# Kernel tuning notes

Measured on AMD Instinct MI355X. Metric: run time of the kernel, lower is better.

Reference implementation:

```python
import jax, jax.numpy as jnp
import numpy as np

EPS = 1e-5  # torch BatchNorm2d default eps


def _conv_bn(x, w, b, gamma, beta, mean, var):
    # 1x1 conv -> relu -> BatchNorm (eval mode, running stats), per Conv2d helper
    y = jnp.einsum('bchw,oc->bohw', x, w) + b[None, :, None, None]
    y = jax.nn.relu(y)
    inv = gamma / jnp.sqrt(var + EPS)
    return y * inv[None, :, None, None] + (beta - mean * inv)[None, :, None, None]


def setup_inputs() -> dict:
    key = jax.random.key(0)
    ks = jax.random.split(key, 32)
    B, C, H, W = 4, 128, 64, 64
    d = {'x': jax.random.normal(ks[0], (B, C, H, W), jnp.float32)}
    i = 1
    for p in ('theta', 'phi', 'g', 'out'):
        d[f'{p}_w'] = jax.random.normal(ks[i], (C, C), jnp.float32) * 0.05; i += 1
        d[f'{p}_b'] = jax.random.normal(ks[i], (C,), jnp.float32) * 0.05; i += 1
        d[f'{p}_gamma'] = jax.random.uniform(ks[i], (C,), jnp.float32, 0.5, 1.5); i += 1
        d[f'{p}_beta'] = jax.random.normal(ks[i], (C,), jnp.float32) * 0.05; i += 1
        d[f'{p}_mean'] = jax.random.normal(ks[i], (C,), jnp.float32) * 0.05; i += 1
        d[f'{p}_var'] = jax.random.uniform(ks[i], (C,), jnp.float32, 0.5, 1.5); i += 1
    return d


def reference(x, theta_w, theta_b, theta_gamma, theta_beta, theta_mean, theta_var,
              phi_w, phi_b, phi_gamma, phi_beta, phi_mean, phi_var,
              g_w, g_b, g_gamma, g_beta, g_mean, g_var,
              out_w, out_b, out_gamma, out_beta, out_mean, out_var):
    B, C, H, W = x.shape
    N = H * W
    # faithful to torch: .view(B, -1, C) is a raw reshape of the (B,C,H,W) buffer
    theta = _conv_bn(x, theta_w, theta_b, theta_gamma, theta_beta, theta_mean, theta_var).reshape(B, N, C)
    phi = _conv_bn(x, phi_w, phi_b, phi_gamma, phi_beta, phi_mean, phi_var).reshape(B, N, C)
    g = _conv_bn(x, g_w, g_b, g_gamma, g_beta, g_mean, g_var).reshape(B, N, C)
    attn = jax.nn.softmax(jnp.einsum('bnc,bmc->bnm', theta, phi), axis=2)  # (B,N,N)
    # Dropout1d is identity in eval mode
    t = jnp.einsum('bnm,bmc->bnc', attn, g).reshape(B, C, H, W)
    t = jnp.einsum('bchw,oc->bohw', t, out_w) + out_b[None, :, None, None]
    inv = out_gamma / jnp.sqrt(out_var + EPS)
    t = t * inv[None, :, None, None] + (out_beta - out_mean * inv)[None, :, None, None]
    t = jax.nn.relu(t)
    return x + t, attn
```

## Files before the change

### kernel.cpp

```cpp
#include <hip/hip_runtime.h>


typedef _Float16 f16;
typedef __attribute__((ext_vector_type(8))) _Float16 f16x8;
typedef __attribute__((ext_vector_type(4))) float f32x4;

#define CC 128
#define NN 4096
#define BB 4
#define NC (NN * CC)
#define EPS_BN 1e-5f

#define OFF_THETA (0ull)
#define OFF_PHI   (4ull << 20)
#define OFF_G     (8ull << 20)
#define OFF_GT    (12ull << 20)
#define OFF_PSTAT (8ull << 20)
#define OFF_TPART (16ull << 20)
#define OFF_T     (32ull << 20)

__global__ __launch_bounds__(256) void k_prep(
    const float* __restrict__ x,
    const float* __restrict__ t_w, const float* __restrict__ t_b,
    const float* __restrict__ t_ga, const float* __restrict__ t_be,
    const float* __restrict__ t_me, const float* __restrict__ t_va,
    const float* __restrict__ p_w, const float* __restrict__ p_b,
    const float* __restrict__ p_ga, const float* __restrict__ p_be,
    const float* __restrict__ p_me, const float* __restrict__ p_va,
    const float* __restrict__ g_w, const float* __restrict__ g_b,
    const float* __restrict__ g_ga, const float* __restrict__ g_be,
    const float* __restrict__ g_me, const float* __restrict__ g_va,
    f16* __restrict__ th, f16* __restrict__ ph, f16* __restrict__ gh)
{
  const int s  = blockIdx.x * 256 + threadIdx.x;
  const int o0 = blockIdx.y * 8;
  const int b  = blockIdx.z;
  const float* xb = x + (size_t)b * NC;

  float acc[3][8];
#pragma unroll
  for (int br = 0; br < 3; ++br)
#pragma unroll
    for (int j = 0; j < 8; ++j) acc[br][j] = 0.f;

#pragma unroll 4
  for (int c = 0; c < CC; ++c) {
    float xv = xb[c * NN + s];
#pragma unroll
    for (int j = 0; j < 8; ++j) {
      acc[0][j] += t_w[(o0 + j) * CC + c] * xv;
      acc[1][j] += p_w[(o0 + j) * CC + c] * xv;
      acc[2][j] += g_w[(o0 + j) * CC + c] * xv;
    }
  }

  f16* outs[3] = { th, ph, gh };
  const float* bi[3] = { t_b,  p_b,  g_b  };
  const float* ga[3] = { t_ga, p_ga, g_ga };
  const float* be[3] = { t_be, p_be, g_be };
  const float* me[3] = { t_me, p_me, g_me };
  const float* va[3] = { t_va, p_va, g_va };
#pragma unroll
  for (int br = 0; br < 3; ++br) {
#pragma unroll
    for (int j = 0; j < 8; ++j) {
      int o = o0 + j;
      float inv = ga[br][o] * rsqrtf(va[br][o] + EPS_BN);
      float add = be[br][o] - me[br][o] * inv;
      float y = fmaxf(acc[br][j] + bi[br][o], 0.f) * inv + add;
      outs[br][(size_t)b * NC + (size_t)o * NN + s] = (f16)y;
    }
  }
}

__global__ __launch_bounds__(256) void k_tr_g(const f16* __restrict__ gh,
                                              f16* __restrict__ gt)
{
  __shared__ f16 tile[64][72];
  const int b   = blockIdx.z;
  const int m0  = blockIdx.x * 64;
  const int c20 = blockIdx.y * 64;
  const f16* gb_ = gh + (size_t)b * NC;
  f16* gtb = gt + (size_t)b * NC;
  const int t = threadIdx.x;
  {
    const int mr = t >> 2, co = (t & 3) * 16;
    f16x8 v0 = *(const f16x8*)(gb_ + (size_t)(m0 + mr) * CC + c20 + co);
    f16x8 v1 = *(const f16x8*)(gb_ + (size_t)(m0 + mr) * CC + c20 + co + 8);
#pragma unroll
    for (int j = 0; j < 8; ++j) tile[co + j][mr] = v0[j];
#pragma unroll
    for (int j = 0; j < 8; ++j) tile[co + 8 + j][mr] = v1[j];
  }
  __syncthreads();
  {
    const int cr = t >> 2, mo = (t & 3) * 16;
    f16x8 w0 = *(const f16x8*)(&tile[cr][mo]);
    f16x8 w1 = *(const f16x8*)(&tile[cr][mo + 8]);
    *(f16x8*)(gtb + (size_t)(c20 + cr) * NN + m0 + mo)     = w0;
    *(f16x8*)(gtb + (size_t)(c20 + cr) * NN + m0 + mo + 8) = w1;
  }
}

__global__ __launch_bounds__(256, 4) void k_sweep1(
    const f16* __restrict__ th, const f16* __restrict__ ph_,
    float2* __restrict__ pstat)
{
  const int bid = blockIdx.x;
  const int b = bid & 3, chunk = (bid >> 2) & 3, rb = bid >> 4;
  const int tid = threadIdx.x, w = tid >> 6;
  const int lane = tid & 63, lr = lane & 15, lg = lane >> 4;
  const int n0 = rb * 128 + w * 32;
  const f16* tb_ = th  + (size_t)b * NC;
  const f16* pb_ = ph_ + (size_t)b * NC;

  f16x8 a[2][4];
#pragma unroll
  for (int tr = 0; tr < 2; ++tr)
#pragma unroll
    for (int kk = 0; kk < 4; ++kk)
      a[tr][kk] = *(const f16x8*)(tb_ + (size_t)(n0 + tr * 16 + lr) * CC + kk * 32 + lg * 8);

  float m[2][4], l[2][4];
#pragma unroll
  for (int tr = 0; tr < 2; ++tr)
#pragma unroll
    for (int r = 0; r < 4; ++r) { m[tr][r] = -1e30f; l[tr][r] = 0.f; }

  const int mbase = chunk * 1024;
#pragma unroll 2
  for (int t = 0; t < 64; ++t) {
    const int mc = mbase + t * 16;
    f16x8 bf[4];
#pragma unroll
    for (int kk = 0; kk < 4; ++kk)
      bf[kk] = *(const f16x8*)(pb_ + (size_t)(mc + lr) * CC + kk * 32 + lg * 8);
#pragma unroll
    for (int tr = 0; tr < 2; ++tr) {
      f32x4 d = {0.f, 0.f, 0.f, 0.f};
#pragma unroll
      for (int kk = 0; kk < 4; ++kk)
        d = __builtin_amdgcn_mfma_f32_16x16x32_f16(a[tr][kk], bf[kk], d, 0, 0, 0);
#pragma unroll
      for (int r = 0; r < 4; ++r) {
        float dd = d[r] - m[tr][r];
        if (dd > 8.f) { l[tr][r] = l[tr][r] * __expf(-dd) + 1.f; m[tr][r] = d[r]; }
        else          { l[tr][r] += __expf(dd); }
      }
    }
  }
#pragma unroll
  for (int off = 1; off < 16; off <<= 1) {
#pragma unroll
    for (int tr = 0; tr < 2; ++tr)
#pragma unroll
      for (int r = 0; r < 4; ++r) {
        float mo = __shfl_xor(m[tr][r], off);
        float lo = __shfl_xor(l[tr][r], off);
        float mn = fmaxf(m[tr][r], mo);
        l[tr][r] = l[tr][r] * __expf(m[tr][r] - mn) + lo * __expf(mo - mn);
        m[tr][r] = mn;
      }
  }
  if (lr == 0) {
#pragma unroll
    for (int tr = 0; tr < 2; ++tr)
#pragma unroll
      for (int r = 0; r < 4; ++r)
        pstat[(size_t)(chunk * BB + b) * NN + n0 + tr * 16 + lg * 4 + r] =
            make_float2(m[tr][r], l[tr][r]);
  }
}

#define LSTR 132

__global__ __launch_bounds__(256, 2) void k_sweep2(
    const f16* __restrict__ th, const f16* __restrict__ ph_,
    const f16* __restrict__ gt, const float2* __restrict__ pstat,
    float* __restrict__ attn, f16* __restrict__ tpart)
{
  __shared__ float plds[4 * 32 * LSTR];
  const int bid = blockIdx.x;
  const int b = bid & 3, chunk = (bid >> 2) & 3, rb = bid >> 4;
  const int tid = threadIdx.x, w = tid >> 6;
  const int lane = tid & 63, lr = lane & 15, lg = lane >> 4;
  const int n0 = rb * 128 + w * 32;
  const f16* tb_ = th  + (size_t)b * NC;
  const f16* pb_ = ph_ + (size_t)b * NC;
  const f16* gb_ = gt  + (size_t)b * NC;
  float* pw = plds + w * 32 * LSTR;

  f16x8 aq[2][4];
#pragma unroll
  for (int tr = 0; tr < 2; ++tr)
#pragma unroll
    for (int kk = 0; kk < 4; ++kk)
      aq[tr][kk] = *(const f16x8*)(tb_ + (size_t)(n0 + tr * 16 + lr) * CC + kk * 32 + lg * 8);

  float S[2][4];
#pragma unroll
  for (int tr = 0; tr < 2; ++tr)
#pragma unroll
    for (int r = 0; r < 4; ++r) {
      const int row = n0 + tr * 16 + lg * 4 + r;
      float mM = -1e30f, LL = 0.f;
#pragma unroll
      for (int ch = 0; ch < 4; ++ch) {
        float2 ps = pstat[(size_t)(ch * BB + b) * NN + row];
        float mn = fmaxf(mM, ps.x);
        LL = LL * __expf(mM - mn) + ps.y * __expf(ps.x - mn);
        mM = mn;
      }
      S[tr][r] = mM + __logf(LL);
    }

  f32x4 tacc[2][8];
#pragma unroll
  for (int tr = 0; tr < 2; ++tr)
#pragma unroll
    for (int ct = 0; ct < 8; ++ct) tacc[tr][ct] = (f32x4){0.f, 0.f, 0.f, 0.f};

  float* attn_b = attn + (size_t)b * NN * NN;
  const int mbase = chunk * 1024;

  for (int blk = 0; blk < 8; ++blk) {
#pragma unroll
    for (int gi = 0; gi < 4; ++gi) {
      const int m0 = mbase + (blk * 4 + gi) * 32;
#pragma unroll
      for (int sub = 0; sub < 2; ++sub) {
        const int mc = m0 + sub * 16;
        f16x8 bf[4];
#pragma unroll
        for (int kk = 0; kk < 4; ++kk)
          bf[kk] = *(const f16x8*)(pb_ + (size_t)(mc + lr) * CC + kk * 32 + lg * 8);
#pragma unroll
        for (int tr = 0; tr < 2; ++tr) {
          f32x4 d = {0.f, 0.f, 0.f, 0.f};
#pragma unroll
          for (int kk = 0; kk < 4; ++kk)
            d = __builtin_amdgcn_mfma_f32_16x16x32_f16(aq[tr][kk], bf[kk], d, 0, 0, 0);
#pragma unroll
          for (int r = 0; r < 4; ++r)
            pw[(tr * 16 + lg * 4 + r) * LSTR + gi * 32 + sub * 16 + lr] =
                __expf(d[r] - S[tr][r]);
        }
      }
      f16x8 pa[2];
#pragma unroll
      for (int tr = 0; tr < 2; ++tr) {
        f32x4 q0 = *(const f32x4*)&pw[(tr * 16 + lr) * LSTR + gi * 32 + lg * 8];
        f32x4 q1 = *(const f32x4*)&pw[(tr * 16 + lr) * LSTR + gi * 32 + lg * 8 + 4];
#pragma unroll
        for (int e = 0; e < 4; ++e) { pa[tr][e] = (f16)q0[e]; pa[tr][4 + e] = (f16)q1[e]; }
      }
#pragma unroll
      for (int ct = 0; ct < 8; ++ct) {
        f16x8 gbf = *(const f16x8*)(gb_ + (size_t)(ct * 16 + lr) * NN + m0 + lg * 8);
#pragma unroll
        for (int tr = 0; tr < 2; ++tr)
          tacc[tr][ct] = __builtin_amdgcn_mfma_f32_16x16x32_f16(pa[tr], gbf, tacc[tr][ct], 0, 0, 0);
      }
    }
    const int fr = lane >> 5, fc = (lane & 31) * 4;
#pragma unroll
    for (int j = 0; j < 32; j += 2) {
      f32x4 v = *(const f32x4*)&pw[(j + fr) * LSTR + fc];
      __builtin_nontemporal_store(v,
          (f32x4*)(attn_b + (size_t)(n0 + j + fr) * NN + mbase + blk * 128 + fc));
    }
  }

  f16* pwh = (f16*)pw;
#pragma unroll
  for (int tr = 0; tr < 2; ++tr)
#pragma unroll
    for (int ct = 0; ct < 8; ++ct)
#pragma unroll
      for (int r = 0; r < 4; ++r)
        pwh[(tr * 16 + lg * 4 + r) * 264 + ct * 16 + lr] = (f16)tacc[tr][ct][r];
  f16* tp = tpart + (size_t)(chunk * BB + b) * NC;
#pragma unroll
  for (int j = 0; j < 32; j += 4) {
    const int row = j + (lane >> 4), colh = (lane & 15) * 8;
    f16x8 v = *(const f16x8*)&pwh[row * 264 + colh];
    *(f16x8*)(tp + (size_t)(n0 + row) * CC + colh) = v;
  }
}

__global__ void k_merge_t(const f16* __restrict__ tpart, f16* __restrict__ t_h)
{
  int i = blockIdx.x * 256 + threadIdx.x;
  size_t base = (size_t)i * 8;
  f16x8 v0 = *(const f16x8*)(tpart + base);
  f16x8 v1 = *(const f16x8*)(tpart + (size_t)BB * NC + base);
  f16x8 v2 = *(const f16x8*)(tpart + (size_t)2 * BB * NC + base);
  f16x8 v3 = *(const f16x8*)(tpart + (size_t)3 * BB * NC + base);
  f16x8 o;
#pragma unroll
  for (int j = 0; j < 8; ++j)
    o[j] = (f16)((float)v0[j] + (float)v1[j] + (float)v2[j] + (float)v3[j]);
  *(f16x8*)(t_h + base) = o;
}

__global__ __launch_bounds__(256) void k_outconv(
    const float* __restrict__ x, const f16* __restrict__ t_h,
    const float* __restrict__ o_w, const float* __restrict__ o_b,
    const float* __restrict__ o_ga, const float* __restrict__ o_be,
    const float* __restrict__ o_me, const float* __restrict__ o_va,
    float* __restrict__ out0)
{
  const int s  = blockIdx.x * 256 + threadIdx.x;
  const int o0 = blockIdx.y * 8;
  const int b  = blockIdx.z;
  const f16* tb_ = t_h + (size_t)b * NC;
  float acc[8];
#pragma unroll
  for (int j = 0; j < 8; ++j) acc[j] = 0.f;

#pragma unroll 4
  for (int c = 0; c < CC; ++c) {
    float tv = (float)tb_[c * NN + s];
#pragma unroll
    for (int j = 0; j < 8; ++j)
      acc[j] += o_w[(o0 + j) * CC + c] * tv;
  }
#pragma unroll
  for (int j = 0; j < 8; ++j) {
    int o = o0 + j;
    float inv = o_ga[o] * rsqrtf(o_va[o] + EPS_BN);
    float add = o_be[o] - o_me[o] * inv;
    float y = fmaxf((acc[j] + o_b[o]) * inv + add, 0.f);
    size_t idx = (size_t)(b * CC + o) * NN + s;
    out0[idx] = x[idx] + y;
  }
}

extern "C" void kernel_launch(void* const* d_in, const int* in_sizes, int n_in,
                              void* d_out, int out_size, void* d_ws, size_t ws_size,
                              hipStream_t stream)
{
  (void)in_sizes; (void)n_in; (void)out_size; (void)ws_size;
  const float* x    = (const float*)d_in[0];
  const float* t_w  = (const float*)d_in[1];
  const float* t_b  = (const float*)d_in[2];
  const float* t_ga = (const float*)d_in[3];
  const float* t_be = (const float*)d_in[4];
  const float* t_me = (const float*)d_in[5];
  const float* t_va = (const float*)d_in[6];
  const float* p_w  = (const float*)d_in[7];
  const float* p_b  = (const float*)d_in[8];
  const float* p_ga = (const float*)d_in[9];
  const float* p_be = (const float*)d_in[10];
  const float* p_me = (const float*)d_in[11];
  const float* p_va = (const float*)d_in[12];
  const float* g_w  = (const float*)d_in[13];
  const float* g_b  = (const float*)d_in[14];
  const float* g_ga = (const float*)d_in[15];
  const float* g_be = (const float*)d_in[16];
  const float* g_me = (const float*)d_in[17];
  const float* g_va = (const float*)d_in[18];
  const float* o_w  = (const float*)d_in[19];
  const float* o_b  = (const float*)d_in[20];
  const float* o_ga = (const float*)d_in[21];
  const float* o_be = (const float*)d_in[22];
  const float* o_me = (const float*)d_in[23];
  const float* o_va = (const float*)d_in[24];

  char* ws = (char*)d_ws;
  f16*    th    = (f16*)   (ws + OFF_THETA);
  f16*    ph    = (f16*)   (ws + OFF_PHI);
  f16*    gh    = (f16*)   (ws + OFF_G);
  f16*    gt    = (f16*)   (ws + OFF_GT);
  float2* pstat = (float2*)(ws + OFF_PSTAT);
  f16*    tpart = (f16*)   (ws + OFF_TPART);
  f16*    t_h   = (f16*)   (ws + OFF_T);

  float* out0 = (float*)d_out;
  float* attn = out0 + (size_t)BB * CC * NN;

  k_prep<<<dim3(16, 16, BB), 256, 0, stream>>>(
      x, t_w, t_b, t_ga, t_be, t_me, t_va,
         p_w, p_b, p_ga, p_be, p_me, p_va,
         g_w, g_b, g_ga, g_be, g_me, g_va, th, ph, gh);
  k_tr_g<<<dim3(64, 2, BB), 256, 0, stream>>>(gh, gt);
  k_sweep1<<<512, 256, 0, stream>>>(th, ph, pstat);
  k_sweep2<<<512, 256, 0, stream>>>(th, ph, gt, pstat, attn, tpart);
  k_merge_t<<<1024, 256, 0, stream>>>(tpart, t_h);
  k_outconv<<<dim3(16, 16, BB), 256, 0, stream>>>(
      x, t_h, o_w, o_b, o_ga, o_be, o_me, o_va, out0);
}
```

Measured before the change: 543.7 us.

## Stage attention probabilities as f16, retile sweep1, fold partial merge into outconv

The partial-sum merge kernel is removed. The out-projection kernel now sums the four chunk partials directly and computes 32 output channels per thread instead of 8. In sweep2 the exponentiated scores are staged in LDS as f16 instead of f32, halving LDS traffic and dropping a conversion. The attention rows are then widened back to f32 for 256-column nontemporal stores. Sweep1 is retiled so each wave handles 64 rows over 512 columns across 8 chunks, raising reuse of the phi loads. The cost is f16 rounding of the attention output values and higher register pressure in outconv and sweep1.

```diff
diff --git a/kernel.cpp b/kernel.cpp
--- a/kernel.cpp
+++ b/kernel.cpp
@@ -2,6 +2,7 @@
 
 
 typedef _Float16 f16;
+typedef __attribute__((ext_vector_type(4))) _Float16 f16x4;
 typedef __attribute__((ext_vector_type(8))) _Float16 f16x8;
 typedef __attribute__((ext_vector_type(4))) float f32x4;
 
@@ -17,7 +18,6 @@
 #define OFF_GT    (12ull << 20)
 #define OFF_PSTAT (8ull << 20)
 #define OFF_TPART (16ull << 20)
-#define OFF_T     (32ull << 20)
 
 __global__ __launch_bounds__(256) void k_prep(
     const float* __restrict__ x,
@@ -102,41 +102,40 @@
   }
 }
 
-__global__ __launch_bounds__(256, 4) void k_sweep1(
+__global__ __launch_bounds__(256, 2) void k_sweep1(
     const f16* __restrict__ th, const f16* __restrict__ ph_,
     float2* __restrict__ pstat)
 {
   const int bid = blockIdx.x;
-  const int b = bid & 3, chunk = (bid >> 2) & 3, rb = bid >> 4;
+  const int b = bid & 3, chunk = (bid >> 2) & 7, rb = bid >> 5;
   const int tid = threadIdx.x, w = tid >> 6;
   const int lane = tid & 63, lr = lane & 15, lg = lane >> 4;
-  const int n0 = rb * 128 + w * 32;
+  const int n0w = rb * 256 + w * 64;
   const f16* tb_ = th  + (size_t)b * NC;
   const f16* pb_ = ph_ + (size_t)b * NC;
 
-  f16x8 a[2][4];
-#pragma unroll
-  for (int tr = 0; tr < 2; ++tr)
+  f16x8 a[4][4];
+#pragma unroll
+  for (int tr = 0; tr < 4; ++tr)
 #pragma unroll
     for (int kk = 0; kk < 4; ++kk)
-      a[tr][kk] = *(const f16x8*)(tb_ + (size_t)(n0 + tr * 16 + lr) * CC + kk * 32 + lg * 8);
-
-  float m[2][4], l[2][4];
-#pragma unroll
-  for (int tr = 0; tr < 2; ++tr)
+      a[tr][kk] = *(const f16x8*)(tb_ + (size_t)(n0w + tr * 16 + lr) * CC + kk * 32 + lg * 8);
+
+  float m[4][4], l[4][4];
+#pragma unroll
+  for (int tr = 0; tr < 4; ++tr)
 #pragma unroll
     for (int r = 0; r < 4; ++r) { m[tr][r] = -1e30f; l[tr][r] = 0.f; }
 
-  const int mbase = chunk * 1024;
-#pragma unroll 2
-  for (int t = 0; t < 64; ++t) {
+  const int mbase = chunk * 512;
+  for (int t = 0; t < 32; ++t) {
     const int mc = mbase + t * 16;
     f16x8 bf[4];
 #pragma unroll
     for (int kk = 0; kk < 4; ++kk)
       bf[kk] = *(const f16x8*)(pb_ + (size_t)(mc + lr) * CC + kk * 32 + lg * 8);
 #pragma unroll
-    for (int tr = 0; tr < 2; ++tr) {
+    for (int tr = 0; tr < 4; ++tr) {
       f32x4 d = {0.f, 0.f, 0.f, 0.f};
 #pragma unroll
       for (int kk = 0; kk < 4; ++kk)
@@ -152,7 +151,7 @@
 #pragma unroll
   for (int off = 1; off < 16; off <<= 1) {
 #pragma unroll
-    for (int tr = 0; tr < 2; ++tr)
+    for (int tr = 0; tr < 4; ++tr)
 #pragma unroll
       for (int r = 0; r < 4; ++r) {
         float mo = __shfl_xor(m[tr][r], off);
@@ -164,48 +163,48 @@
   }
   if (lr == 0) {
 #pragma unroll
-    for (int tr = 0; tr < 2; ++tr)
+    for (int tr = 0; tr < 4; ++tr)
 #pragma unroll
       for (int r = 0; r < 4; ++r)
-        pstat[(size_t)(chunk * BB + b) * NN + n0 + tr * 16 + lg * 4 + r] =
+        pstat[(size_t)(chunk * BB + b) * NN + n0w + tr * 16 + lg * 4 + r] =
             make_float2(m[tr][r], l[tr][r]);
   }
 }
 
-#define LSTR 132
+#define WSTR 264
 
 __global__ __launch_bounds__(256, 2) void k_sweep2(
     const f16* __restrict__ th, const f16* __restrict__ ph_,
     const f16* __restrict__ gt, const float2* __restrict__ pstat,
     float* __restrict__ attn, f16* __restrict__ tpart)
 {
-  __shared__ float plds[4 * 32 * LSTR];
+  __shared__ f16 plds[4 * 32 * WSTR];
   const int bid = blockIdx.x;
   const int b = bid & 3, chunk = (bid >> 2) & 3, rb = bid >> 4;
   const int tid = threadIdx.x, w = tid >> 6;
   const int lane = tid & 63, lr = lane & 15, lg = lane >> 4;
-  const int n0 = rb * 128 + w * 32;
+  const int n0w = rb * 128 + w * 32;
   const f16* tb_ = th  + (size_t)b * NC;
   const f16* pb_ = ph_ + (size_t)b * NC;
   const f16* gb_ = gt  + (size_t)b * NC;
-  float* pw = plds + w * 32 * LSTR;
+  f16* pw = plds + w * 32 * WSTR;
 
   f16x8 aq[2][4];
 #pragma unroll
   for (int tr = 0; tr < 2; ++tr)
 #pragma unroll
     for (int kk = 0; kk < 4; ++kk)
-      aq[tr][kk] = *(const f16x8*)(tb_ + (size_t)(n0 + tr * 16 + lr) * CC + kk * 32 + lg * 8);
+      aq[tr][kk] = *(const f16x8*)(tb_ + (size_t)(n0w + tr * 16 + lr) * CC + kk * 32 + lg * 8);
 
   float S[2][4];
 #pragma unroll
   for (int tr = 0; tr < 2; ++tr)
 #pragma unroll
     for (int r = 0; r < 4; ++r) {
-      const int row = n0 + tr * 16 + lg * 4 + r;
+      const int row = n0w + tr * 16 + lg * 4 + r;
       float mM = -1e30f, LL = 0.f;
 #pragma unroll
-      for (int ch = 0; ch < 4; ++ch) {
+      for (int ch = 0; ch < 8; ++ch) {
         float2 ps = pstat[(size_t)(ch * BB + b) * NN + row];
         float mn = fmaxf(mM, ps.x);
         LL = LL * __expf(mM - mn) + ps.y * __expf(ps.x - mn);
@@ -223,10 +222,10 @@
   float* attn_b = attn + (size_t)b * NN * NN;
   const int mbase = chunk * 1024;
 
-  for (int blk = 0; blk < 8; ++blk) {
-#pragma unroll
-    for (int gi = 0; gi < 4; ++gi) {
-      const int m0 = mbase + (blk * 4 + gi) * 32;
+  for (int win = 0; win < 4; ++win) {
+#pragma unroll
+    for (int gi = 0; gi < 8; ++gi) {
+      const int m0 = mbase + win * 256 + gi * 32;
 #pragma unroll
       for (int sub = 0; sub < 2; ++sub) {
         const int mc = m0 + sub * 16;
@@ -242,18 +241,14 @@
             d = __builtin_amdgcn_mfma_f32_16x16x32_f16(aq[tr][kk], bf[kk], d, 0, 0, 0);
 #pragma unroll
           for (int r = 0; r < 4; ++r)
-            pw[(tr * 16 + lg * 4 + r) * LSTR + gi * 32 + sub * 16 + lr] =
-                __expf(d[r] - S[tr][r]);
+            pw[(tr * 16 + lg * 4 + r) * WSTR + gi * 32 + sub * 16 + lr] =
+                (f16)__expf(d[r] - S[tr][r]);
         }
       }
       f16x8 pa[2];
 #pragma unroll
-      for (int tr = 0; tr < 2; ++tr) {
-        f32x4 q0 = *(const f32x4*)&pw[(tr * 16 + lr) * LSTR + gi * 32 + lg * 8];
-        f32x4 q1 = *(const f32x4*)&pw[(tr * 16 + lr) * LSTR + gi * 32 + lg * 8 + 4];
-#pragma unroll
-        for (int e = 0; e < 4; ++e) { pa[tr][e] = (f16)q0[e]; pa[tr][4 + e] = (f16)q1[e]; }
-      }
+      for (int tr = 0; tr < 2; ++tr)
+        pa[tr] = *(const f16x8*)&pw[(tr * 16 + lr) * WSTR + gi * 32 + lg * 8];
 #pragma unroll
       for (int ct = 0; ct < 8; ++ct) {
         f16x8 gbf = *(const f16x8*)(gb_ + (size_t)(ct * 16 + lr) * NN + m0 + lg * 8);
@@ -262,71 +257,62 @@
           tacc[tr][ct] = __builtin_amdgcn_mfma_f32_16x16x32_f16(pa[tr], gbf, tacc[tr][ct], 0, 0, 0);
       }
     }
-    const int fr = lane >> 5, fc = (lane & 31) * 4;
-#pragma unroll
-    for (int j = 0; j < 32; j += 2) {
-      f32x4 v = *(const f32x4*)&pw[(j + fr) * LSTR + fc];
-      __builtin_nontemporal_store(v,
-          (f32x4*)(attn_b + (size_t)(n0 + j + fr) * NN + mbase + blk * 128 + fc));
-    }
-  }
-
-  f16* pwh = (f16*)pw;
+    const int wcol = mbase + win * 256;
+#pragma unroll 8
+    for (int j = 0; j < 32; ++j) {
+      f16x4 v = *(const f16x4*)&pw[j * WSTR + lane * 4];
+      f32x4 o = { (float)v[0], (float)v[1], (float)v[2], (float)v[3] };
+      __builtin_nontemporal_store(o,
+          (f32x4*)(attn_b + (size_t)(n0w + j) * NN + wcol + lane * 4));
+    }
+    asm volatile("s_waitcnt lgkmcnt(0)" ::: "memory");
+  }
+
 #pragma unroll
   for (int tr = 0; tr < 2; ++tr)
 #pragma unroll
     for (int ct = 0; ct < 8; ++ct)
 #pragma unroll
       for (int r = 0; r < 4; ++r)
-        pwh[(tr * 16 + lg * 4 + r) * 264 + ct * 16 + lr] = (f16)tacc[tr][ct][r];
+        pw[(tr * 16 + lg * 4 + r) * WSTR + ct * 16 + lr] = (f16)tacc[tr][ct][r];
   f16* tp = tpart + (size_t)(chunk * BB + b) * NC;
-#pragma unroll
-  for (int j = 0; j < 32; j += 4) {
-    const int row = j + (lane >> 4), colh = (lane & 15) * 8;
-    f16x8 v = *(const f16x8*)&pwh[row * 264 + colh];
-    *(f16x8*)(tp + (size_t)(n0 + row) * CC + colh) = v;
-  }
-}
-
-__global__ void k_merge_t(const f16* __restrict__ tpart, f16* __restrict__ t_h)
-{
-  int i = blockIdx.x * 256 + threadIdx.x;
-  size_t base = (size_t)i * 8;
-  f16x8 v0 = *(const f16x8*)(tpart + base);
-  f16x8 v1 = *(const f16x8*)(tpart + (size_t)BB * NC + base);
-  f16x8 v2 = *(const f16x8*)(tpart + (size_t)2 * BB * NC + base);
-  f16x8 v3 = *(const f16x8*)(tpart + (size_t)3 * BB * NC + base);
-  f16x8 o;
-#pragma unroll
-  for (int j = 0; j < 8; ++j)
-    o[j] = (f16)((float)v0[j] + (float)v1[j] + (float)v2[j] + (float)v3[j]);
-  *(f16x8*)(t_h + base) = o;
+  const int frow = lane >> 4, fcol = (lane & 15) * 8;
+#pragma unroll
+  for (int j = 0; j < 8; ++j) {
+    const int row = j * 4 + frow;
+    f16x8 v = *(const f16x8*)&pw[row * WSTR + fcol];
+    *(f16x8*)(tp + (size_t)(n0w + row) * CC + fcol) = v;
+  }
 }
 
 __global__ __launch_bounds__(256) void k_outconv(
-    const float* __restrict__ x, const f16* __restrict__ t_h,
+    const float* __restrict__ x, const f16* __restrict__ tpart,
     const float* __restrict__ o_w, const float* __restrict__ o_b,
     const float* __restrict__ o_ga, const float* __restrict__ o_be,
     const float* __restrict__ o_me, const float* __restrict__ o_va,
     float* __restrict__ out0)
 {
   const int s  = blockIdx.x * 256 + threadIdx.x;
-  const int o0 = blockIdx.y * 8;
+  const int o0 = blockIdx.y * 32;
   const int b  = blockIdx.z;
-  const f16* tb_ = t_h + (size_t)b * NC;
-  float acc[8];
-#pragma unroll
-  for (int j = 0; j < 8; ++j) acc[j] = 0.f;
-
-#pragma unroll 4
+  const f16* tb_ = tpart + (size_t)b * NC;
+  float acc[32];
+#pragma unroll
+  for (int j = 0; j < 32; ++j) acc[j] = 0.f;
+
+#pragma unroll 2
   for (int c = 0; c < CC; ++c) {
-    float tv = (float)tb_[c * NN + s];
-#pragma unroll
-    for (int j = 0; j < 8; ++j)
+    const size_t idx = (size_t)c * NN + s;
+    float tv = (float)tb_[idx] +
+               (float)tb_[(size_t)BB * NC + idx] +
+               (float)tb_[(size_t)2 * BB * NC + idx] +
+               (float)tb_[(size_t)3 * BB * NC + idx];
+#pragma unroll
+    for (int j = 0; j < 32; ++j)
       acc[j] += o_w[(o0 + j) * CC + c] * tv;
   }
 #pragma unroll
-  for (int j = 0; j < 8; ++j) {
+  for (int j = 0; j < 32; ++j) {
     int o = o0 + j;
     float inv = o_ga[o] * rsqrtf(o_va[o] + EPS_BN);
     float add = o_be[o] - o_me[o] * inv;
@@ -374,7 +360,6 @@
   f16*    gt    = (f16*)   (ws + OFF_GT);
   float2* pstat = (float2*)(ws + OFF_PSTAT);
   f16*    tpart = (f16*)   (ws + OFF_TPART);
-  f16*    t_h   = (f16*)   (ws + OFF_T);
 
   float* out0 = (float*)d_out;
   float* attn = out0 + (size_t)BB * CC * NN;
@@ -382,11 +367,10 @@
   k_prep<<<dim3(16, 16, BB), 256, 0, stream>>>(
       x, t_w, t_b, t_ga, t_be, t_me, t_va,
          p_w, p_b, p_ga, p_be, p_me, p_va,
-         g_w, g_b, g_ga, g_be, g_me, g_va, th, ph, gh);
+         g_w, g_b, g_ga, g_me == g_me ? g_be : g_be, g_me, g_va, th, ph, gh);
   k_tr_g<<<dim3(64, 2, BB), 256, 0, stream>>>(gh, gt);
   k_sweep1<<<512, 256, 0, stream>>>(th, ph, pstat);
   k_sweep2<<<512, 256, 0, stream>>>(th, ph, gt, pstat, attn, tpart);
-  k_merge_t<<<1024, 256, 0, stream>>>(tpart, t_h);
-  k_outconv<<<dim3(16, 16, BB), 256, 0, stream>>>(
-      x, t_h, o_w, o_b, o_ga, o_be, o_me, o_va, out0);
-}
+  k_outconv<<<dim3(16, 4, BB), 256, 0, stream>>>(
+      x, tpart, o_w, o_b, o_ga, o_be, o_me, o_va, out0);
+}
```

Result: slower. 558.6 us (+2.7%).
